# Optimization experiments

Hardware: AMD Instinct MI355X
Metric: run time of the kernel (lower is better)

The kernel has to match this reference:

```python
import jax, jax.numpy as jnp
import numpy as np

B, T, D = 16, 2048, 1024


def setup_inputs() -> dict:
    key = jax.random.key(0)
    ks = jax.random.split(key, 7)
    s = 1.0 / np.sqrt(D)  # nn.Linear default init bound
    u = lambda k, shape: jax.random.uniform(k, shape, jnp.float32, -s, s)
    return {
        "x": jax.random.normal(ks[0], (B, T, D), jnp.float32),
        "h0": jnp.zeros((B, D), jnp.float32),
        "W_in": u(ks[1], (2 * D, D)),
        "b_in": u(ks[2], (2 * D,)),
        "W_dt": u(ks[3], (D, D)),
        "b_dt": u(ks[4], (D,)),
        "W_out": u(ks[5], (D, D)),
        "b_out": u(ks[6], (D,)),
    }


def reference(x, h0, W_in, b_in, W_dt, b_dt, W_out, b_out):
    # in_proj then chunk: first half x_part, second half gate
    xz = jnp.einsum("btd,ed->bte", x, W_in) + b_in          # [B,T,2D]
    x_part, gate = jnp.split(xz, 2, axis=-1)                  # each [B,T,D]
    dt = jax.nn.sigmoid(jnp.einsum("btd,ed->bte", x_part, W_dt) + b_dt)  # [B,T,D]

    def step(h, inp):
        dt_t, xp_t = inp                                      # [B,D] each
        h = (1.0 - dt_t) * h + dt_t * xp_t                    # gated EMA update
        return h, h

    _, hs = jax.lax.scan(step, h0,
                         (jnp.swapaxes(dt, 0, 1), jnp.swapaxes(x_part, 0, 1)))
    hs = jnp.swapaxes(hs, 0, 1)                               # [B,T,D]
    y = jnp.einsum("btd,ed->bte", hs * jax.nn.sigmoid(gate), W_out) + b_out
    return y
```

## Files before the change

### kernel.cpp

```cpp
#include <hip/hip_runtime.h>
#include <hip/hip_bf16.h>
#include <cstdint>

typedef __attribute__((ext_vector_type(8))) short short8;
typedef __attribute__((ext_vector_type(4))) float f32x4;
typedef __attribute__((ext_vector_type(8))) unsigned short ushort8;

#define B_ 16
#define T_ 2048
#define D_ 1024
#define M_ (B_*T_)
#define NC 32
#define CL 64

static __device__ __forceinline__ float bf2f(unsigned short u) {
  unsigned int x = ((unsigned int)u) << 16;
  return __builtin_bit_cast(float, x);
}
static __device__ __forceinline__ unsigned short f2bf(float f) {
  unsigned int x = __builtin_bit_cast(unsigned int, f);
  unsigned int r = x + 0x7fffu + ((x >> 16) & 1u);
  return (unsigned short)(r >> 16);
}
static __device__ __forceinline__ float sigmoidf(float v) {
  return 1.f / (1.f + __expf(-v));
}

typedef const __attribute__((address_space(1))) unsigned int* gas1_t;
typedef __attribute__((address_space(3))) unsigned int* las3_t;
static __device__ __forceinline__ void async_copy16(const void* g, void* l) {
  __builtin_amdgcn_global_load_lds((gas1_t)g, (las3_t)l, 16, 0, 0);
}

#define VMCNT4 asm volatile("s_waitcnt vmcnt(4)" ::: "memory")
#define VMCNT2 asm volatile("s_waitcnt vmcnt(2)" ::: "memory")
#define VMCNT0 asm volatile("s_waitcnt vmcnt(0)" ::: "memory")
#define SBAR   __builtin_amdgcn_s_barrier()
#define SCHED0 __builtin_amdgcn_sched_barrier(0)

__global__ void cvt_f32_bf16(const float* __restrict__ in,
                             unsigned short* __restrict__ out, long n8) {
  long i = (long)blockIdx.x * blockDim.x + threadIdx.x;
  long stride = (long)gridDim.x * blockDim.x;
  for (; i < n8; i += stride) {
    const float4* p = (const float4*)(in + i * 8);
    float4 a = p[0], b = p[1];
    ushort8 o;
    o[0] = f2bf(a.x); o[1] = f2bf(a.y); o[2] = f2bf(a.z); o[3] = f2bf(a.w);
    o[4] = f2bf(b.x); o[5] = f2bf(b.y); o[6] = f2bf(b.z); o[7] = f2bf(b.w);
    *(ushort8*)(out + i * 8) = o;
  }
}

template<int EPI>
__global__ __launch_bounds__(512, 2) void gemm256(
    const unsigned short* __restrict__ A, long lda,
    const unsigned short* __restrict__ Bw,
    const float* __restrict__ bias,
    void* __restrict__ Cout, long ldc,
    int nbx)
{
  constexpr int KT = 16;
  __shared__ __align__(16) unsigned short lds[65536];

  const int tid = threadIdx.x;
  const int l  = tid & 63, w = tid >> 6;
  const int wm = w >> 2, wn = w & 3;
  const int fr = l & 15, g = l >> 4;
  const int t8 = tid >> 3;
  const int c8x = ((l & 7) ^ (l >> 3)) << 4;
  const int s0 = ((g ^ (fr & 7)) << 4);
  const int s1 = s0 ^ 0x40;
  const int tB = (w >> 2) * 64 + (w & 3) * 8 + (l >> 3);

  const int nwg = gridDim.x;
  const int cpx = nwg >> 3;
  const int bid = blockIdx.x;
  const int swz = (bid & 7) * cpx + (bid >> 3);
  const long m0 = (long)(swz / nbx) * 256;
  const long n0 = (long)(swz % nbx) * 256;

  const char* Ab = (const char*)A;
  const char* Bb = (const char*)Bw;
  const long ldab = lda * 2;
  char* LB = (char*)lds;

  auto stA = [&](int kt, int h, int nb) {
    char* lb = LB + nb * 32768 + h * 16384 + w * 1024;
    long col = (long)kt * 128 + c8x;
    async_copy16(Ab + (m0 + h * 64 + t8) * ldab + col, lb);
    async_copy16(Ab + (m0 + 128 + h * 64 + t8) * ldab + col, lb + 8192);
  };
  auto stB = [&](int kt, int h, int nb) {
    char* lb = LB + 65536 + nb * 32768 + h * 16384 + w * 1024;
    long col = (long)kt * 128 + c8x;
    async_copy16(Bb + (n0 + tB + h * 32) * 2048 + col, lb);
    async_copy16(Bb + (n0 + tB + 128 + h * 32) * 2048 + col, lb + 8192);
  };

  f32x4 acc[8][4] = {};

  stA(0, 0, 0); stB(0, 0, 0); stB(0, 1, 0); stA(0, 1, 0);
  VMCNT4; SCHED0; SBAR;

#define PH(mh, nh, STG, VMW) do {                                              \
    const char* pa0 = LB + cur * 32768 + (mh) * 16384 + wm * 8192 + fr * 128 + s0; \
    const char* pa1 = LB + cur * 32768 + (mh) * 16384 + wm * 8192 + fr * 128 + s1; \
    const char* pb0 = LB + 65536 + cur * 32768 + (nh) * 16384 + wn * 4096 + fr * 128 + s0; \
    const char* pb1 = LB + 65536 + cur * 32768 + (nh) * 16384 + wn * 4096 + fr * 128 + s1; \
    short8 af[4][2]; short8 bf[2][2];                                          \
    _Pragma("unroll") for (int mi = 0; mi < 4; ++mi) {                         \
      af[mi][0] = *(const short8*)(pa0 + mi * 2048);                           \
      af[mi][1] = *(const short8*)(pa1 + mi * 2048); }                         \
    _Pragma("unroll") for (int ni = 0; ni < 2; ++ni) {                         \
      bf[ni][0] = *(const short8*)(pb0 + ni * 2048);                           \
      bf[ni][1] = *(const short8*)(pb1 + ni * 2048); }                         \
    STG;                                                                       \
    SCHED0; SBAR;                                                              \
    __builtin_amdgcn_s_setprio(1);                                             \
    _Pragma("unroll") for (int mi = 0; mi < 4; ++mi)                           \
    _Pragma("unroll") for (int ni = 0; ni < 2; ++ni) {                         \
      acc[(mh)*4+mi][(nh)*2+ni] = __builtin_amdgcn_mfma_f32_16x16x32_bf16(     \
          af[mi][0], bf[ni][0], acc[(mh)*4+mi][(nh)*2+ni], 0, 0, 0);           \
      acc[(mh)*4+mi][(nh)*2+ni] = __builtin_amdgcn_mfma_f32_16x16x32_bf16(     \
          af[mi][1], bf[ni][1], acc[(mh)*4+mi][(nh)*2+ni], 0, 0, 0); }         \
    __builtin_amdgcn_s_setprio(0);                                             \
    VMW;                                                                       \
    SCHED0; SBAR; SCHED0;                                                      \
  } while (0)

#pragma unroll 2
  for (int t = 0; t < KT; ++t) {
    const int cur = t & 1, nxt = cur ^ 1;
    const bool notlast = (t + 1 < KT);
    PH(0, 0, if (notlast) stA(t + 1, 0, nxt), { if (notlast) { VMCNT4; } else { VMCNT2; } });
    PH(0, 1, if (notlast) stB(t + 1, 0, nxt), { if (notlast) { VMCNT4; } else { VMCNT0; } });
    PH(1, 0, if (notlast) stB(t + 1, 1, nxt), {});
    PH(1, 1, if (notlast) stA(t + 1, 1, nxt), { if (notlast) { VMCNT4; } });
  }
#undef PH

  const int rq = l >> 4;
#pragma unroll
  for (int mi = 0; mi < 8; ++mi) {
    long row0 = m0 + wm * 128 + mi * 16 + rq * 4;
#pragma unroll
    for (int ni = 0; ni < 4; ++ni) {
      long col = n0 + wn * 64 + ni * 16 + fr;
      float bv = bias[col];
#pragma unroll
      for (int r = 0; r < 4; ++r) {
        float v = acc[mi][ni][r] + bv;
        if (EPI == 1) v = sigmoidf(v);
        if (EPI == 2) {
          ((float*)Cout)[(row0 + r) * ldc + col] = v;
        } else {
          ((unsigned short*)Cout)[(row0 + r) * ldc + col] = f2bf(v);
        }
      }
    }
  }
}

__global__ void scan_passA(const unsigned short* __restrict__ dtb,
                           const unsigned short* __restrict__ xz,
                           float* __restrict__ P, float* __restrict__ Hl)
{
  int idx = blockIdx.x * blockDim.x + threadIdx.x;
  int d8 = idx & 127;
  int c  = (idx >> 7) & 31;
  int b  = idx >> 12;
  int d0 = d8 * 8;
  long mbase = (long)b * T_ + (long)c * CL;
  float h[8] = {0,0,0,0,0,0,0,0};
  float p[8] = {1,1,1,1,1,1,1,1};
  for (int t = 0; t < CL; ++t) {
    long m = mbase + t;
    ushort8 dv = *(const ushort8*)(dtb + m * D_ + d0);
    ushort8 xv = *(const ushort8*)(xz + m * (2 * D_) + d0);
#pragma unroll
    for (int j = 0; j < 8; ++j) {
      float dt = bf2f(dv[j]);
      float xp = bf2f(xv[j]);
      float om = 1.f - dt;
      h[j] = om * h[j] + dt * xp;
      p[j] *= om;
    }
  }
  long pb = ((long)(b * NC + c)) * D_ + d0;
#pragma unroll
  for (int j = 0; j < 8; ++j) { P[pb + j] = p[j]; Hl[pb + j] = h[j]; }
}

__global__ void scan_passC(unsigned short* dts,
                           const unsigned short* __restrict__ xz,
                           const float* __restrict__ h0,
                           const float* __restrict__ P,
                           const float* __restrict__ Hl)
{
  int idx = blockIdx.x * blockDim.x + threadIdx.x;
  int d8 = idx & 127;
  int c  = (idx >> 7) & 31;
  int b  = idx >> 12;
  int d0 = d8 * 8;
  long mbase = (long)b * T_ + (long)c * CL;

  float h[8];
#pragma unroll
  for (int j = 0; j < 8; ++j) h[j] = h0[(long)b * D_ + d0 + j];

  for (int jc = 0; jc < c; ++jc) {
    long pb = ((long)(b * NC + jc)) * D_ + d0;
    float pj[8], hj[8];
    *(f32x4*)&pj[0] = *(const f32x4*)(P + pb);
    *(f32x4*)&pj[4] = *(const f32x4*)(P + pb + 4);
    *(f32x4*)&hj[0] = *(const f32x4*)(Hl + pb);
    *(f32x4*)&hj[4] = *(const f32x4*)(Hl + pb + 4);
#pragma unroll
    for (int j = 0; j < 8; ++j) h[j] = hj[j] + pj[j] * h[j];
  }

  for (int t = 0; t < CL; ++t) {
    long m = mbase + t;
    ushort8 dv = *(const ushort8*)(dts + m * D_ + d0);
    ushort8 xv = *(const ushort8*)(xz + m * (2 * D_) + d0);
    ushort8 gv = *(const ushort8*)(xz + m * (2 * D_) + D_ + d0);
    ushort8 ov;
#pragma unroll
    for (int j = 0; j < 8; ++j) {
      float dt = bf2f(dv[j]);
      float xp = bf2f(xv[j]);
      h[j] = (1.f - dt) * h[j] + dt * xp;
      float gt = bf2f(gv[j]);
      ov[j] = f2bf(h[j] * sigmoidf(gt));
    }
    *(ushort8*)(dts + m * D_ + d0) = ov;
  }
}

extern "C" void kernel_launch(void* const* d_in, const int* in_sizes, int n_in,
                              void* d_out, int out_size, void* d_ws, size_t ws_size,
                              hipStream_t stream) {
  const float* x     = (const float*)d_in[0];
  const float* h0    = (const float*)d_in[1];
  const float* W_in  = (const float*)d_in[2];
  const float* b_in  = (const float*)d_in[3];
  const float* W_dt  = (const float*)d_in[4];
  const float* b_dt  = (const float*)d_in[5];
  const float* W_out = (const float*)d_in[6];
  const float* b_out = (const float*)d_in[7];
  float* out = (float*)d_out;

  char* ws = (char*)d_ws;
  const size_t OFF_XB    = 0;
  const size_t OFF_WIN   = 67108864;
  const size_t OFF_WDT   = 71303168;
  const size_t OFF_WOUT  = 73400320;
  const size_t OFF_XZ    = 75497472;
  const size_t OFF_DTS   = 209715200;
  const size_t OFF_P     = 276824064;
  const size_t OFF_HL    = 278921216;
  const size_t NEEDED    = 281018368;
  if (ws_size < NEEDED) return;

  unsigned short* xb    = (unsigned short*)(ws + OFF_XB);
  unsigned short* wbin  = (unsigned short*)(ws + OFF_WIN);
  unsigned short* wbdt  = (unsigned short*)(ws + OFF_WDT);
  unsigned short* wbout = (unsigned short*)(ws + OFF_WOUT);
  unsigned short* xz    = (unsigned short*)(ws + OFF_XZ);
  unsigned short* dts   = (unsigned short*)(ws + OFF_DTS);
  float* P  = (float*)(ws + OFF_P);
  float* Hl = (float*)(ws + OFF_HL);

  cvt_f32_bf16<<<2048, 256, 0, stream>>>(x, xb, (long)M_ * D_ / 8);
  cvt_f32_bf16<<<512, 256, 0, stream>>>(W_in, wbin, (long)2 * D_ * D_ / 8);
  cvt_f32_bf16<<<256, 256, 0, stream>>>(W_dt, wbdt, (long)D_ * D_ / 8);
  cvt_f32_bf16<<<256, 256, 0, stream>>>(W_out, wbout, (long)D_ * D_ / 8);

  gemm256<0><<<(M_/256)*(2*D_/256), 512, 0, stream>>>(xb, D_, wbin, b_in, xz, 2*D_, 2*D_/256);
  gemm256<1><<<(M_/256)*(D_/256), 512, 0, stream>>>(xz, 2*D_, wbdt, b_dt, dts, D_, D_/256);
  scan_passA<<<256, 256, 0, stream>>>(dts, xz, P, Hl);
  scan_passC<<<256, 256, 0, stream>>>(dts, xz, h0, P, Hl);
  gemm256<2><<<(M_/256)*(D_/256), 512, 0, stream>>>(dts, D_, wbout, b_out, out, D_, D_/256);
}
```

Baseline: 464.7 us.

## Stage GEMM epilogue through swizzled LDS, reuse fragments across phases, fuse weight casts

The GEMM epilogue now writes each wave's accumulator tile into XOR-swizzled shared memory and then emits 16-byte vectorized global stores, replacing scattered 2/4-byte stores. The main loop is restructured so A/B fragments loaded in one phase are reused by the next, cutting LDS reads per K-step from 4 A+4 B reads to fewer. The three weight conversion launches are merged into one kernel. This adds LDS traffic and barriers in the epilogue and drops the unroll-2 pragma.

```diff
diff --git a/kernel.cpp b/kernel.cpp
--- a/kernel.cpp
+++ b/kernel.cpp
@@ -35,6 +35,7 @@
 #define VMCNT4 asm volatile("s_waitcnt vmcnt(4)" ::: "memory")
 #define VMCNT2 asm volatile("s_waitcnt vmcnt(2)" ::: "memory")
 #define VMCNT0 asm volatile("s_waitcnt vmcnt(0)" ::: "memory")
+#define LGKM0  asm volatile("s_waitcnt lgkmcnt(0)" ::: "memory")
 #define SBAR   __builtin_amdgcn_s_barrier()
 #define SCHED0 __builtin_amdgcn_sched_barrier(0)
 
@@ -50,6 +51,22 @@
     o[4] = f2bf(b.x); o[5] = f2bf(b.y); o[6] = f2bf(b.z); o[7] = f2bf(b.w);
     *(ushort8*)(out + i * 8) = o;
   }
+}
+
+__global__ void cvt_w3(const float* __restrict__ w1, unsigned short* __restrict__ o1,
+                       const float* __restrict__ w2, unsigned short* __restrict__ o2,
+                       const float* __restrict__ w3, unsigned short* __restrict__ o3) {
+  long i = (long)blockIdx.x * blockDim.x + threadIdx.x;
+  const float* src; unsigned short* dst; long off;
+  if (i < 262144)      { src = w1; dst = o1; off = i; }
+  else if (i < 393216) { src = w2; dst = o2; off = i - 262144; }
+  else                 { src = w3; dst = o3; off = i - 393216; }
+  const float4* p = (const float4*)(src + off * 8);
+  float4 a = p[0], b = p[1];
+  ushort8 o;
+  o[0] = f2bf(a.x); o[1] = f2bf(a.y); o[2] = f2bf(a.z); o[3] = f2bf(a.w);
+  o[4] = f2bf(b.x); o[5] = f2bf(b.y); o[6] = f2bf(b.z); o[7] = f2bf(b.w);
+  *(ushort8*)(dst + off * 8) = o;
 }
 
 template<int EPI>
@@ -100,64 +117,124 @@
 
   f32x4 acc[8][4] = {};
 
-  stA(0, 0, 0); stB(0, 0, 0); stB(0, 1, 0); stA(0, 1, 0);
+  stA(0, 0, 0); stB(0, 0, 0); stA(0, 1, 0); stB(0, 1, 0);
   VMCNT4; SCHED0; SBAR;
 
-#define PH(mh, nh, STG, VMW) do {                                              \
-    const char* pa0 = LB + cur * 32768 + (mh) * 16384 + wm * 8192 + fr * 128 + s0; \
-    const char* pa1 = LB + cur * 32768 + (mh) * 16384 + wm * 8192 + fr * 128 + s1; \
-    const char* pb0 = LB + 65536 + cur * 32768 + (nh) * 16384 + wn * 4096 + fr * 128 + s0; \
-    const char* pb1 = LB + 65536 + cur * 32768 + (nh) * 16384 + wn * 4096 + fr * 128 + s1; \
-    short8 af[4][2]; short8 bf[2][2];                                          \
+#define RD_A(DST, MH) do {                                                     \
+    const char* p0_ = LB + cur * 32768 + (MH) * 16384 + wm * 8192 + fr * 128 + s0; \
+    const char* p1_ = LB + cur * 32768 + (MH) * 16384 + wm * 8192 + fr * 128 + s1; \
     _Pragma("unroll") for (int mi = 0; mi < 4; ++mi) {                         \
-      af[mi][0] = *(const short8*)(pa0 + mi * 2048);                           \
-      af[mi][1] = *(const short8*)(pa1 + mi * 2048); }                         \
+      DST[mi][0] = *(const short8*)(p0_ + mi * 2048);                          \
+      DST[mi][1] = *(const short8*)(p1_ + mi * 2048); }                        \
+  } while (0)
+#define RD_B(DST, NH) do {                                                     \
+    const char* p0_ = LB + 65536 + cur * 32768 + (NH) * 16384 + wn * 4096 + fr * 128 + s0; \
+    const char* p1_ = LB + 65536 + cur * 32768 + (NH) * 16384 + wn * 4096 + fr * 128 + s1; \
     _Pragma("unroll") for (int ni = 0; ni < 2; ++ni) {                         \
-      bf[ni][0] = *(const short8*)(pb0 + ni * 2048);                           \
-      bf[ni][1] = *(const short8*)(pb1 + ni * 2048); }                         \
-    STG;                                                                       \
-    SCHED0; SBAR;                                                              \
+      DST[ni][0] = *(const short8*)(p0_ + ni * 2048);                          \
+      DST[ni][1] = *(const short8*)(p1_ + ni * 2048); }                        \
+  } while (0)
+#define MM(AF, BF, MB, NB) do {                                                \
     __builtin_amdgcn_s_setprio(1);                                             \
     _Pragma("unroll") for (int mi = 0; mi < 4; ++mi)                           \
     _Pragma("unroll") for (int ni = 0; ni < 2; ++ni) {                         \
-      acc[(mh)*4+mi][(nh)*2+ni] = __builtin_amdgcn_mfma_f32_16x16x32_bf16(     \
-          af[mi][0], bf[ni][0], acc[(mh)*4+mi][(nh)*2+ni], 0, 0, 0);           \
-      acc[(mh)*4+mi][(nh)*2+ni] = __builtin_amdgcn_mfma_f32_16x16x32_bf16(     \
-          af[mi][1], bf[ni][1], acc[(mh)*4+mi][(nh)*2+ni], 0, 0, 0); }         \
+      acc[(MB)+mi][(NB)+ni] = __builtin_amdgcn_mfma_f32_16x16x32_bf16(         \
+          AF[mi][0], BF[ni][0], acc[(MB)+mi][(NB)+ni], 0, 0, 0);               \
+      acc[(MB)+mi][(NB)+ni] = __builtin_amdgcn_mfma_f32_16x16x32_bf16(         \
+          AF[mi][1], BF[ni][1], acc[(MB)+mi][(NB)+ni], 0, 0, 0); }             \
     __builtin_amdgcn_s_setprio(0);                                             \
-    VMW;                                                                       \
-    SCHED0; SBAR; SCHED0;                                                      \
   } while (0)
 
-#pragma unroll 2
   for (int t = 0; t < KT; ++t) {
     const int cur = t & 1, nxt = cur ^ 1;
     const bool notlast = (t + 1 < KT);
-    PH(0, 0, if (notlast) stA(t + 1, 0, nxt), { if (notlast) { VMCNT4; } else { VMCNT2; } });
-    PH(0, 1, if (notlast) stB(t + 1, 0, nxt), { if (notlast) { VMCNT4; } else { VMCNT0; } });
-    PH(1, 0, if (notlast) stB(t + 1, 1, nxt), {});
-    PH(1, 1, if (notlast) stA(t + 1, 1, nxt), { if (notlast) { VMCNT4; } });
-  }
-#undef PH
-
+    short8 af0[4][2], af1[4][2], bf0[2][2], bf1[2][2];
+    RD_A(af0, 0); RD_B(bf0, 0);
+    if (notlast) stA(t + 1, 0, nxt);
+    SCHED0; SBAR;
+    MM(af0, bf0, 0, 0);
+    if (notlast) { VMCNT4; } else { VMCNT2; }
+    SCHED0; SBAR; SCHED0;
+    RD_A(af1, 1);
+    if (notlast) stB(t + 1, 0, nxt);
+    SCHED0; SBAR;
+    MM(af1, bf0, 4, 0);
+    if (notlast) { VMCNT4; } else { VMCNT0; }
+    SCHED0; SBAR; SCHED0;
+    RD_B(bf1, 1);
+    if (notlast) stA(t + 1, 1, nxt);
+    SCHED0; SBAR;
+    MM(af1, bf1, 4, 2);
+    SCHED0; SBAR; SCHED0;
+    RD_A(af0, 0);
+    if (notlast) stB(t + 1, 1, nxt);
+    SCHED0; SBAR;
+    MM(af0, bf1, 0, 2);
+    if (notlast) { VMCNT4; }
+    SCHED0; SBAR; SCHED0;
+  }
+#undef RD_A
+#undef RD_B
+#undef MM
+
+  __syncthreads();
+
+  char* ep = LB + w * 16384;
   const int rq = l >> 4;
-#pragma unroll
-  for (int mi = 0; mi < 8; ++mi) {
-    long row0 = m0 + wm * 128 + mi * 16 + rq * 4;
-#pragma unroll
-    for (int ni = 0; ni < 4; ++ni) {
-      long col = n0 + wn * 64 + ni * 16 + fr;
-      float bv = bias[col];
-#pragma unroll
-      for (int r = 0; r < 4; ++r) {
-        float v = acc[mi][ni][r] + bv;
-        if (EPI == 1) v = sigmoidf(v);
-        if (EPI == 2) {
-          ((float*)Cout)[(row0 + r) * ldc + col] = v;
-        } else {
-          ((unsigned short*)Cout)[(row0 + r) * ldc + col] = f2bf(v);
+  if (EPI != 2) {
+#pragma unroll
+    for (int mi = 0; mi < 8; ++mi)
+#pragma unroll
+      for (int ni = 0; ni < 4; ++ni) {
+        int cl = ni * 16 + fr;
+        float bv = bias[n0 + wn * 64 + cl];
+#pragma unroll
+        for (int r = 0; r < 4; ++r) {
+          float v = acc[mi][ni][r] + bv;
+          if (EPI == 1) v = sigmoidf(v);
+          int row = mi * 16 + rq * 4 + r;
+          int byte = (row * 128 + cl * 2) ^ ((row & 7) << 4);
+          *(unsigned short*)(ep + byte) = f2bf(v);
         }
       }
+    LGKM0; SCHED0;
+#pragma unroll
+    for (int i = 0; i < 16; ++i) {
+      int row = i * 8 + (l >> 3);
+      int cb = (l & 7) * 16;
+      int byte = (row * 128 + cb) ^ ((row & 7) << 4);
+      short8 v = *(const short8*)(ep + byte);
+      *(short8*)((unsigned short*)Cout + (m0 + wm * 128 + row) * ldc
+                 + n0 + wn * 64 + (cb >> 1)) = v;
+    }
+  } else {
+#pragma unroll
+    for (int p = 0; p < 2; ++p) {
+#pragma unroll
+      for (int mi = 0; mi < 4; ++mi)
+#pragma unroll
+        for (int ni = 0; ni < 4; ++ni) {
+          int cl = ni * 16 + fr;
+          float bv = bias[n0 + wn * 64 + cl];
+#pragma unroll
+          for (int r = 0; r < 4; ++r) {
+            float v = acc[p * 4 + mi][ni][r] + bv;
+            int row = mi * 16 + rq * 4 + r;
+            int byte = (row * 256 + cl * 4) ^ ((row & 7) << 4);
+            *(float*)(ep + byte) = v;
+          }
+        }
+      LGKM0; SCHED0;
+#pragma unroll
+      for (int i = 0; i < 16; ++i) {
+        int row = i * 4 + (l >> 4);
+        int cb = (l & 15) * 16;
+        int byte = (row * 256 + cb) ^ ((row & 7) << 4);
+        f32x4 v = *(const f32x4*)(ep + byte);
+        *(f32x4*)((float*)Cout + (m0 + wm * 128 + p * 64 + row) * ldc
+                  + n0 + wn * 64 + (cb >> 2)) = v;
+      }
+      LGKM0; SCHED0;
     }
   }
 }
@@ -273,9 +350,7 @@
   float* Hl = (float*)(ws + OFF_HL);
 
   cvt_f32_bf16<<<2048, 256, 0, stream>>>(x, xb, (long)M_ * D_ / 8);
-  cvt_f32_bf16<<<512, 256, 0, stream>>>(W_in, wbin, (long)2 * D_ * D_ / 8);
-  cvt_f32_bf16<<<256, 256, 0, stream>>>(W_dt, wbdt, (long)D_ * D_ / 8);
-  cvt_f32_bf16<<<256, 256, 0, stream>>>(W_out, wbout, (long)D_ * D_ / 8);
+  cvt_w3<<<2048, 256, 0, stream>>>(W_in, wbin, W_dt, wbdt, W_out, wbout);
 
   gemm256<0><<<(M_/256)*(2*D_/256), 512, 0, stream>>>(xb, D_, wbin, b_in, xz, 2*D_, 2*D_/256);
   gemm256<1><<<(M_/256)*(D_/256), 512, 0, stream>>>(xz, 2*D_, wbdt, b_dt, dts, D_, D_/256);
```

Result: faster. 446.7 us (-3.9%).
